# Optimization experiments

Measured on AMD Instinct MI355X. Metric: run time of the kernel, lower is better.

The kernel has to match this reference:

```python
import jax, jax.numpy as jnp
from jax import lax
import numpy as np

D_MODEL = 128
N_HEADS = 8
N_POINTS = 8
MAX_MAG = 10.0
NEG_SLOPE = 0.1


def conv2d(x, w, b, pad):
    # x: (N, Cin, H, W), w: (Cout, Cin, kh, kw)
    y = lax.conv_general_dilated(x, w, (1, 1), [(pad, pad), (pad, pad)],
                                 dimension_numbers=('NCHW', 'OIHW', 'NCHW'))
    return y + b[None, :, None, None]


def leaky(x):
    return jnp.where(x >= 0, x, NEG_SLOPE * x)


def bilinear_sample(img, grid):
    # img: (B, C, H, W); grid: (B, P, H, W, 2) in [-1, 1] (x, y)
    # Matches torch F.grid_sample(mode='bilinear', padding_mode='zeros', align_corners=False)
    B, C, H, W = img.shape
    x = ((grid[..., 0] + 1.0) * W - 1.0) * 0.5
    y = ((grid[..., 1] + 1.0) * H - 1.0) * 0.5
    x0 = jnp.floor(x)
    y0 = jnp.floor(y)
    wx1 = x - x0
    wy1 = y - y0

    def one(img_b, x0b, y0b, wx1b, wy1b):
        def gather(xi, yi):
            valid = (xi >= 0) & (xi < W) & (yi >= 0) & (yi < H)
            xc = jnp.clip(xi, 0, W - 1).astype(jnp.int32)
            yc = jnp.clip(yi, 0, H - 1).astype(jnp.int32)
            v = img_b[:, yc, xc]  # (C, P, H, W)
            return v * valid
        wx0b = 1.0 - wx1b
        wy0b = 1.0 - wy1b
        v00 = gather(x0b, y0b)
        v01 = gather(x0b + 1, y0b)
        v10 = gather(x0b, y0b + 1)
        v11 = gather(x0b + 1, y0b + 1)
        return (v00 * (wx0b * wy0b) + v01 * (wx1b * wy0b)
                + v10 * (wx0b * wy1b) + v11 * (wx1b * wy1b))

    return jax.vmap(one)(img, x0, y0, wx1, wy1)  # (B, C, P, H, W)


def ss_deform_attn(value, loc):
    # value: (N, nh, d, H, W); loc: (N, nh, P, H, W, 2) in normalized [0,1] coords
    N, nh, d, H, W = value.shape
    P = loc.shape[2]
    v = value.reshape(N * nh, d, H, W)
    grids = (2.0 * loc - 1.0).reshape(N * nh, P, H, W, 2)
    sampled = bilinear_sample(v, grids)  # (N*nh, d, P, H, W)
    # per-location attention logits = <sampled_point, value_at_location>
    scores = jnp.einsum('ndphw,ndhw->nphw', sampled, v)
    aw = jax.nn.softmax(scores, axis=1)
    out = jnp.einsum('ndphw,nphw->ndhw', sampled, aw)
    return out.reshape(N, nh * d, H, W)


def _forward(query, value, reference_points, co_w1, co_b1, co_w2, co_b2,
             co_w3, co_b3, co_w4, co_b4, val_w, val_b, out_w, out_b):
    N, C, H, W = value.shape
    v = conv2d(value, val_w, val_b, 0)
    v = v.reshape(N, N_HEADS, D_MODEL // N_HEADS, H, W)
    o = leaky(conv2d(query, co_w1, co_b1, 1))
    o = leaky(conv2d(o, co_w2, co_b2, 1))
    o = leaky(conv2d(o, co_w3, co_b3, 1))
    o = conv2d(o, co_w4, co_b4, 1)
    o = MAX_MAG * jnp.tanh(o)
    offsets = o.reshape(N, N_HEADS, N_POINTS, H, W, 2)
    norm = jnp.array([W, H], dtype=o.dtype)  # (x, y) normalizer
    loc = reference_points[:, None, None, :, :, :] + offsets / norm
    out = ss_deform_attn(v, loc)
    return conv2d(out, out_w, out_b, 0)


def setup_inputs() -> dict:
    key = jax.random.key(0)
    ks = jax.random.split(key, 12)
    N, H, W = 4, 80, 80

    def w_init(k, shape):
        fan_in = shape[1] * shape[2] * shape[3]
        return jax.random.normal(k, shape, jnp.float32) / np.sqrt(fan_in)

    return {
        'query': jax.random.normal(ks[0], (N, 2 * D_MODEL, H, W), jnp.float32),
        'value': jax.random.normal(ks[1], (N, D_MODEL, H, W), jnp.float32),
        'reference_points': jax.random.uniform(ks[2], (N, H, W, 2), jnp.float32),
        'co_w1': w_init(ks[3], (D_MODEL, 2 * D_MODEL, 3, 3)),
        'co_b1': jnp.zeros((D_MODEL,), jnp.float32),
        'co_w2': w_init(ks[4], (D_MODEL, D_MODEL, 3, 3)),
        'co_b2': jnp.zeros((D_MODEL,), jnp.float32),
        'co_w3': w_init(ks[5], (D_MODEL, D_MODEL, 3, 3)),
        'co_b3': jnp.zeros((D_MODEL,), jnp.float32),
        'co_w4': w_init(ks[6], (N_HEADS * N_POINTS * 2, D_MODEL, 3, 3)),
        'co_b4': jnp.zeros((N_HEADS * N_POINTS * 2,), jnp.float32),
        'val_w': w_init(ks[7], (D_MODEL, D_MODEL, 1, 1)),
        'val_b': jnp.zeros((D_MODEL,), jnp.float32),
        'out_w': w_init(ks[8], (D_MODEL, D_MODEL, 1, 1)),
        'out_b': jnp.zeros((D_MODEL,), jnp.float32),
    }


def reference(query, value, reference_points, co_w1, co_b1, co_w2, co_b2,
              co_w3, co_b3, co_w4, co_b4, val_w, val_b, out_w, out_b):
    return _forward(query, value, reference_points, co_w1, co_b1, co_w2, co_b2,
                    co_w3, co_b3, co_w4, co_b4, val_w, val_b, out_w, out_b)
```

## Files before the change

### kernel.cpp

```cpp
#include <hip/hip_runtime.h>
#include <math.h>

#define Hh 80
#define Ww 80
#define HW 6400
#define PS 6724
#define NB 4

typedef _Float16 half8 __attribute__((ext_vector_type(8)));
typedef _Float16 half4v __attribute__((ext_vector_type(4)));
typedef float f32x16 __attribute__((ext_vector_type(16)));

__device__ inline void wblob_one(const float* src, _Float16* dst, int CI, int d) {
    int NC = CI / 32;
    int j = d & 7;
    int l = (d >> 3) & 63;
    int h = (d >> 9) & 1;
    int rest = d >> 10;
    int tap = rest % 9;
    rest /= 9;
    int c = rest % NC;
    int CT = rest / NC;
    int co = CT * 32 + (l & 31);
    int ci = c * 32 + h * 16 + (l >> 5) * 8 + j;
    dst[d] = (_Float16)src[((size_t)co * CI + ci) * 9 + tap];
}

__device__ inline void wblob1x1_one(const float* src, _Float16* dst, int d) {
    int j = d & 7;
    int l = (d >> 3) & 63;
    int c = (d >> 9) & 7;
    int CT = d >> 12;
    int co = CT * 32 + (l & 31);
    int ci = c * 16 + (l >> 5) * 8 + j;
    dst[d] = (_Float16)src[co * 128 + ci];
}

__device__ inline int padsite(int p) {
    if (p < 82) return p;
    if (p < 164) return 81 * 82 + (p - 82);
    if (p < 244) return (p - 163) * 82;
    return (p - 243) * 82 + 81;
}

__global__ void prep_kernel(const float* __restrict__ w1, const float* __restrict__ w2,
                            const float* __restrict__ w3, const float* __restrict__ w4,
                            const float* __restrict__ vw, const float* __restrict__ ow,
                            _Float16* __restrict__ b1, _Float16* __restrict__ b2,
                            _Float16* __restrict__ b3, _Float16* __restrict__ b4,
                            _Float16* __restrict__ bv, _Float16* __restrict__ bo,
                            int* __restrict__ qh_i, int* __restrict__ hA_i,
                            int* __restrict__ hB_i) {
    int idx = blockIdx.x * 256 + threadIdx.x;
    if (idx < 294912) { wblob_one(w1, b1, 256, idx); return; }
    idx -= 294912;
    if (idx < 147456) { wblob_one(w2, b2, 128, idx); return; }
    idx -= 147456;
    if (idx < 147456) { wblob_one(w3, b3, 128, idx); return; }
    idx -= 147456;
    if (idx < 147456) { wblob_one(w4, b4, 128, idx); return; }
    idx -= 147456;
    if (idx < 16384) { wblob1x1_one(vw, bv, idx); return; }
    idx -= 16384;
    if (idx < 16384) { wblob1x1_one(ow, bo, idx); return; }
    idx -= 16384;
    if (idx < 165888) {
        int n = idx / 41472, rr = idx % 41472;
        int c = rr / 5184, r2 = rr % 5184;
        int p = r2 >> 4, k = r2 & 15;
        qh_i[((size_t)(n * 8 + c) * PS + padsite(p)) * 16 + k] = 0;
        return;
    }
    idx -= 165888;
    if (idx < 82944) {
        int n = idx / 20736, rr = idx % 20736;
        int c = rr / 5184, r2 = rr % 5184;
        int p = r2 >> 4, k = r2 & 15;
        hA_i[((size_t)(n * 4 + c) * PS + padsite(p)) * 16 + k] = 0;
        return;
    }
    idx -= 82944;
    if (idx < 82944) {
        int n = idx / 20736, rr = idx % 20736;
        int c = rr / 5184, r2 = rr % 5184;
        int p = r2 >> 4, k = r2 & 15;
        hB_i[((size_t)(n * 4 + c) * PS + padsite(p)) * 16 + k] = 0;
    }
}

__global__ __launch_bounds__(256) void q_transpose(
    const float* __restrict__ in, _Float16* __restrict__ out) {
    const int b = blockIdx.x;
    const int xcd = b & 7, n = xcd & 3, hi = xcd >> 2;
    const int s0 = hi * 3200 + (b >> 3) * 64;
    const int t = threadIdx.x;
    constexpr int CI = 256, ST = CI + 8;
    __shared__ _Float16 T[64 * ST];
    for (int idx = t; idx < 64 * CI; idx += 256) {
        int ci = idx >> 6, sl = idx & 63;
        T[sl * ST + ci] = (_Float16)in[((size_t)n * CI + ci) * HW + s0 + sl];
    }
    __syncthreads();
    for (int idx = t; idx < 64 * 32; idx += 256) {
        int q = idx & 31, sl = idx >> 5;
        int s = s0 + sl, yy = s / 80, xx = s % 80;
        int c = q >> 2, off = (q & 3) * 8;
        *(int4*)(out + ((size_t)(n * 8 + c) * PS + (yy + 1) * 82 + (xx + 1)) * 32 + off) =
            *(const int4*)(&T[sl * ST + q * 8]);
    }
}

__global__ __launch_bounds__(256) void v_transpose(
    const float* __restrict__ in, _Float16* __restrict__ out) {
    const int b = blockIdx.x;
    const int xcd = b & 7, n = xcd & 3, hi = xcd >> 2;
    const int s0 = hi * 3200 + (b >> 3) * 64;
    const int t = threadIdx.x;
    constexpr int CI = 128, ST = CI + 8;
    __shared__ _Float16 T[64 * ST];
    for (int idx = t; idx < 64 * CI; idx += 256) {
        int ci = idx >> 6, sl = idx & 63;
        T[sl * ST + ci] = (_Float16)in[((size_t)n * CI + ci) * HW + s0 + sl];
    }
    __syncthreads();
    for (int idx = t; idx < 64 * 16; idx += 256) {
        int q = idx & 15, sl = idx >> 4;
        *(int4*)(out + ((size_t)n * HW + s0 + sl) * CI + q * 8) =
            *(const int4*)(&T[sl * ST + q * 8]);
    }
}

template <int NCp, int ACT>
__global__ __launch_bounds__(256) void conv3x3_mfma(
    const _Float16* __restrict__ in, const _Float16* __restrict__ wblob,
    const float* __restrict__ bias, void* __restrict__ outp) {
    constexpr int NS = NCp * 18;
    const int b = blockIdx.x;
    const int xcd = b & 7, n = xcd & 3, hi = xcd >> 2;
    const int r = b >> 3;
    const int coH = r & 1, j = r >> 1;
    const int x0 = (j % 5) * 16, y0 = hi * 40 + (j / 5) * 8;
    const int t = threadIdx.x;
    const int w = t >> 6, l = t & 63;
    const int x0w = x0 + (w & 1) * 8, y0w = y0 + (w >> 1) * 4;
    const int lane31 = l & 31, lhalf = l >> 5;
    const int lx = lane31 & 7, ly = lane31 >> 3;

    const _Float16* p0 = in + ((size_t)(n * NCp) * PS + (y0w + ly + 1) * 82 + (x0w + lx + 1)) * 32 + lhalf * 8;
    const _Float16* wA0 = wblob + ((size_t)(coH * 2) * NS) * 512 + l * 8;
    const _Float16* wA1 = wA0 + (size_t)NS * 512;

    f32x16 acc0 = {}, acc1 = {};
    half8 bB[9], bA0[9], bA1[9];

    auto boff = [](int t2) -> size_t {
        int c = t2 / 18, u = t2 % 18;
        int tap = u >> 1, h = u & 1;
        int dy = tap / 3, dx = tap % 3;
        return (size_t)c * (PS * 32) + ((dy - 1) * 82 + (dx - 1)) * 32 + h * 16;
    };

#pragma unroll
    for (int t2 = 0; t2 < 9; ++t2) {
        bB[t2]  = *(const half8*)(p0 + boff(t2));
        bA0[t2] = *(const half8*)(wA0 + t2 * 512);
        bA1[t2] = *(const half8*)(wA1 + t2 * 512);
    }

#pragma unroll
    for (int t2 = 0; t2 < NS; ++t2) {
        const int slot = t2 % 9;
        acc0 = __builtin_amdgcn_mfma_f32_32x32x16_f16(bA0[slot], bB[slot], acc0, 0, 0, 0);
        acc1 = __builtin_amdgcn_mfma_f32_32x32x16_f16(bA1[slot], bB[slot], acc1, 0, 0, 0);
        if (t2 + 9 < NS) {
            const int t2p = t2 + 9;
            bB[slot]  = *(const half8*)(p0 + boff(t2p));
            bA0[slot] = *(const half8*)(wA0 + (size_t)t2p * 512);
            bA1[slot] = *(const half8*)(wA1 + (size_t)t2p * 512);
        }
    }

    const int y = y0w + ly, x = x0w + lx;
#pragma unroll
    for (int ct = 0; ct < 2; ++ct) {
        const f32x16& acc = ct ? acc1 : acc0;
#pragma unroll
        for (int q = 0; q < 4; ++q) {
            const int inner = 8 * q + 4 * lhalf;
            const int co0 = coH * 64 + ct * 32 + inner;
            float v[4];
#pragma unroll
            for (int i = 0; i < 4; ++i) {
                float vv = acc[q * 4 + i] + bias[co0 + i];
                if (ACT == 1) vv = (vv >= 0.f) ? vv : 0.1f * vv;
                else vv = 10.f * tanhf(vv);
                v[i] = vv;
            }
            if (ACT == 1) {
                half4v hv = {(_Float16)v[0], (_Float16)v[1], (_Float16)v[2], (_Float16)v[3]};
                const int c2 = coH * 2 + ct;
                *(half4v*)((_Float16*)outp +
                    ((size_t)(n * 4 + c2) * PS + (y + 1) * 82 + (x + 1)) * 32 + inner) = hv;
            } else {
                float4 fv = {v[0], v[1], v[2], v[3]};
                *(float4*)((float*)outp + ((size_t)n * HW + y * 80 + x) * 128 + co0) = fv;
            }
        }
    }
}

template <int MODE>
__global__ __launch_bounds__(256) void conv1x1_mfma(
    const _Float16* __restrict__ in, const _Float16* __restrict__ wblob,
    const float* __restrict__ bias, float* __restrict__ outp) {
    const int b = blockIdx.x;
    const int xcd = b & 7, n = xcd & 3, hi = xcd >> 2;
    const int r = b >> 3;
    const int coH = r & 1, strip = r >> 1;
    const int t = threadIdx.x;
    const int w = t >> 6, l = t & 63;
    const int lane31 = l & 31, lhalf = l >> 5;
    const int s = hi * 3200 + strip * 128 + w * 32 + lane31;

    const _Float16* pB = in + (size_t)(n * HW + s) * 128 + lhalf * 8;
    const _Float16* pA0 = wblob + (size_t)(coH * 2) * 8 * 512 + l * 8;
    const _Float16* pA1 = pA0 + 8 * 512;

    half8 bB[8], bA0[8], bA1[8];
#pragma unroll
    for (int c = 0; c < 8; ++c) {
        bB[c]  = *(const half8*)(pB + c * 16);
        bA0[c] = *(const half8*)(pA0 + (size_t)c * 512);
        bA1[c] = *(const half8*)(pA1 + (size_t)c * 512);
    }
    f32x16 acc0 = {}, acc1 = {};
#pragma unroll
    for (int c = 0; c < 8; ++c) {
        acc0 = __builtin_amdgcn_mfma_f32_32x32x16_f16(bA0[c], bB[c], acc0, 0, 0, 0);
        acc1 = __builtin_amdgcn_mfma_f32_32x32x16_f16(bA1[c], bB[c], acc1, 0, 0, 0);
    }

#pragma unroll
    for (int ct = 0; ct < 2; ++ct) {
        const f32x16& acc = ct ? acc1 : acc0;
#pragma unroll
        for (int q = 0; q < 4; ++q) {
            const int co0 = coH * 64 + ct * 32 + 8 * q + 4 * lhalf;
            if (MODE == 0) {
                const int hd = co0 >> 4, dd = co0 & 15;
                float4 fv = {acc[4 * q + 0] + bias[co0 + 0], acc[4 * q + 1] + bias[co0 + 1],
                             acc[4 * q + 2] + bias[co0 + 2], acc[4 * q + 3] + bias[co0 + 3]};
                *(float4*)&outp[((size_t)(n * 8 + hd) * HW + s) * 16 + dd] = fv;
            } else {
#pragma unroll
                for (int i = 0; i < 4; ++i)
                    outp[(size_t)(n * 128 + co0 + i) * HW + s] = acc[4 * q + i] + bias[co0 + i];
            }
        }
    }
}

__global__ __launch_bounds__(256, 2) void deform_attn_kernel(
    const float* __restrict__ v_s, const float* __restrict__ offs,
    const float* __restrict__ ref, _Float16* __restrict__ att) {
    const int slice = blockIdx.x;
    const int n = slice >> 3, hd = slice & 7;
    const int t = threadIdx.x;
    const int s = blockIdx.y * 64 + (t >> 2);
    const int d0 = (t & 3) * 4;
    const int nb = n * 8 + hd;
    const float* vbase = v_s + (size_t)nb * (HW * 16) + d0;

    const float4 cv = *(const float4*)&v_s[((size_t)nb * HW + s) * 16 + d0];
    const float rx = ref[(size_t)(n * HW + s) * 2 + 0] * 80.f - 0.5f;
    const float ry = ref[(size_t)(n * HW + s) * 2 + 1] * 80.f - 0.5f;

    const int e = (s >= 3200) ? 1 : 0;
    const float* ob0 = offs + ((size_t)n * HW + (2 * s - e * HW)) * 128 + hd * 16 + e;

    float4 oxv[4], oyv[4];
#pragma unroll
    for (int i = 0; i < 4; ++i) {
        oxv[i] = *(const float4*)(ob0 + i * 4);
        oyv[i] = *(const float4*)(ob0 + 128 + i * 4);
    }
    float ox[8], oy[8];
#pragma unroll
    for (int i = 0; i < 4; ++i) {
        ox[2 * i] = oxv[i].x; ox[2 * i + 1] = oxv[i].z;
        oy[2 * i] = oyv[i].x; oy[2 * i + 1] = oyv[i].z;
    }

    float wx1[8], wy1[8];
    int ix[8], iy[8];
#pragma unroll
    for (int p = 0; p < 8; ++p) {
        const float px = rx + ox[p];
        const float py = ry + oy[p];
        const float fx = floorf(px), fy = floorf(py);
        ix[p] = (int)fx; iy[p] = (int)fy;
        wx1[p] = px - fx; wy1[p] = py - fy;
    }

    float4 g[8][4];
#pragma unroll
    for (int p = 0; p < 8; ++p) {
        const int xc0 = min(max(ix[p], 0), 79),     xc1 = min(max(ix[p] + 1, 0), 79);
        const int yc0 = min(max(iy[p], 0), 79),     yc1 = min(max(iy[p] + 1, 0), 79);
        const int r0 = yc0 * 80, r1 = yc1 * 80;
        g[p][0] = *(const float4*)(vbase + (size_t)(r0 + xc0) * 16);
        g[p][1] = *(const float4*)(vbase + (size_t)(r0 + xc1) * 16);
        g[p][2] = *(const float4*)(vbase + (size_t)(r1 + xc0) * 16);
        g[p][3] = *(const float4*)(vbase + (size_t)(r1 + xc1) * 16);
    }

    float4 sampled[8];
    float score[8];
#pragma unroll
    for (int p = 0; p < 8; ++p) {
        const float vx0 = (ix[p] >= 0 && ix[p] < Ww) ? 1.f : 0.f;
        const float vx1 = (ix[p] + 1 >= 0 && ix[p] + 1 < Ww) ? 1.f : 0.f;
        const float vy0 = (iy[p] >= 0 && iy[p] < Hh) ? 1.f : 0.f;
        const float vy1 = (iy[p] + 1 >= 0 && iy[p] + 1 < Hh) ? 1.f : 0.f;
        const float wx0 = 1.f - wx1[p], wy0 = 1.f - wy1[p];
        const float w00 = wx0 * wy0 * vx0 * vy0;
        const float w01 = wx1[p] * wy0 * vx1 * vy0;
        const float w10 = wx0 * wy1[p] * vx0 * vy1;
        const float w11 = wx1[p] * wy1[p] * vx1 * vy1;
        float4 sv;
        sv.x = g[p][0].x * w00 + g[p][1].x * w01 + g[p][2].x * w10 + g[p][3].x * w11;
        sv.y = g[p][0].y * w00 + g[p][1].y * w01 + g[p][2].y * w10 + g[p][3].y * w11;
        sv.z = g[p][0].z * w00 + g[p][1].z * w01 + g[p][2].z * w10 + g[p][3].z * w11;
        sv.w = g[p][0].w * w00 + g[p][1].w * w01 + g[p][2].w * w10 + g[p][3].w * w11;
        sampled[p] = sv;
        float sc = sv.x * cv.x + sv.y * cv.y + sv.z * cv.z + sv.w * cv.w;
        sc += __shfl_xor(sc, 1);
        sc += __shfl_xor(sc, 2);
        score[p] = sc;
    }

    float m = score[0];
#pragma unroll
    for (int p = 1; p < 8; ++p) m = fmaxf(m, score[p]);
    float sum = 0.f, aw[8];
#pragma unroll
    for (int p = 0; p < 8; ++p) {
        aw[p] = __expf(score[p] - m);
        sum += aw[p];
    }
    const float inv = 1.f / sum;
    float4 o = {0.f, 0.f, 0.f, 0.f};
#pragma unroll
    for (int p = 0; p < 8; ++p) {
        o.x += aw[p] * sampled[p].x;
        o.y += aw[p] * sampled[p].y;
        o.z += aw[p] * sampled[p].z;
        o.w += aw[p] * sampled[p].w;
    }
    o.x *= inv; o.y *= inv; o.z *= inv; o.w *= inv;

    half4v hv = {(_Float16)o.x, (_Float16)o.y, (_Float16)o.z, (_Float16)o.w};
    *(half4v*)&att[((size_t)n * HW + s) * 128 + hd * 16 + d0] = hv;
}

extern "C" void kernel_launch(void* const* d_in, const int* in_sizes, int n_in,
                              void* d_out, int out_size, void* d_ws, size_t ws_size,
                              hipStream_t stream) {
    const float* query = (const float*)d_in[0];
    const float* value = (const float*)d_in[1];
    const float* ref   = (const float*)d_in[2];
    const float* co_w1 = (const float*)d_in[3];
    const float* co_b1 = (const float*)d_in[4];
    const float* co_w2 = (const float*)d_in[5];
    const float* co_b2 = (const float*)d_in[6];
    const float* co_w3 = (const float*)d_in[7];
    const float* co_b3 = (const float*)d_in[8];
    const float* co_w4 = (const float*)d_in[9];
    const float* co_b4 = (const float*)d_in[10];
    const float* val_w = (const float*)d_in[11];
    const float* val_b = (const float*)d_in[12];
    const float* out_w = (const float*)d_in[13];
    const float* out_b = (const float*)d_in[14];

    char* ws = (char*)d_ws;
    size_t o = 0;
    auto alloc = [&](size_t bytes) { char* p = ws + o; o += (bytes + 255) & ~(size_t)255; return p; };

    _Float16* wb2 = (_Float16*)alloc(147456 * 2);
    _Float16* wb3 = (_Float16*)alloc(147456 * 2);
    _Float16* wb4 = (_Float16*)alloc(147456 * 2);
    _Float16* wbv = (_Float16*)alloc(16384 * 2);
    _Float16* wbo = (_Float16*)alloc(16384 * 2);
    char* vsR = alloc(3276800 * 4);
    float* v_s = (float*)vsR;
    _Float16* wb1 = (_Float16*)vsR;
    _Float16* v_h = (_Float16*)alloc((size_t)NB * HW * 128 * 2);
    char* R1 = alloc((size_t)NB * 8 * PS * 32 * 2);
    _Float16* q_h = (_Float16*)R1;
    float* o4 = (float*)R1;
    char* R2 = alloc((size_t)NB * 4 * PS * 32 * 2 * 2);
    _Float16* hA = (_Float16*)R2;
    _Float16* hB = (_Float16*)(R2 + (size_t)NB * 4 * PS * 32 * 2);
    _Float16* att_h = (_Float16*)R2;

    prep_kernel<<<4304, 256, 0, stream>>>(co_w1, co_w2, co_w3, co_w4, val_w, out_w,
                                          wb1, wb2, wb3, wb4, wbv, wbo,
                                          (int*)q_h, (int*)hA, (int*)hB);

    q_transpose<<<400, 256, 0, stream>>>(query, q_h);
    v_transpose<<<400, 256, 0, stream>>>(value, v_h);

    conv3x3_mfma<8, 1><<<400, 256, 0, stream>>>(q_h, wb1, co_b1, hA);

    conv1x1_mfma<0><<<400, 256, 0, stream>>>(v_h, wbv, val_b, v_s);

    conv3x3_mfma<4, 1><<<400, 256, 0, stream>>>(hA, wb2, co_b2, hB);
    conv3x3_mfma<4, 1><<<400, 256, 0, stream>>>(hB, wb3, co_b3, hA);
    conv3x3_mfma<4, 2><<<400, 256, 0, stream>>>(hA, wb4, co_b4, o4);

    deform_attn_kernel<<<dim3(32, 100), 256, 0, stream>>>(v_s, o4, ref, att_h);

    conv1x1_mfma<1><<<400, 256, 0, stream>>>(att_h, wbo, out_b, (float*)d_out);
}
```

Baseline: 266.9 us.

## Stage conv3x3 weights and input halo in LDS via async global_load_lds double-buffering

Restructures the 3x3 conv MFMA kernel so each block covers all 128 output channels for a 16x4 pixel tile. Weights and a halo'd input tile are staged into shared memory with direct global-to-LDS loads, double-buffered per channel group. Previously each wave loaded its operands straight from global memory into registers, which meant redundant input reads across the split output-channel halves. The change adds LDS traffic and a barrier per tap group, and sets a two-blocks-per-CU occupancy hint.

```diff
diff --git a/kernel.cpp b/kernel.cpp
--- a/kernel.cpp
+++ b/kernel.cpp
@@ -10,6 +10,12 @@
 typedef _Float16 half8 __attribute__((ext_vector_type(8)));
 typedef _Float16 half4v __attribute__((ext_vector_type(4)));
 typedef float f32x16 __attribute__((ext_vector_type(16)));
+
+__device__ __forceinline__ void gload16(const _Float16* g, _Float16* l) {
+    __builtin_amdgcn_global_load_lds(
+        (const __attribute__((address_space(1))) void*)g,
+        (__attribute__((address_space(3))) void*)l, 16, 0, 0);
+}
 
 __device__ inline void wblob_one(const float* src, _Float16* dst, int CI, int d) {
     int NC = CI / 32;
@@ -131,63 +137,92 @@
 }
 
 template <int NCp, int ACT>
-__global__ __launch_bounds__(256) void conv3x3_mfma(
+__global__ __launch_bounds__(256, 2) void conv3x3_mfma(
     const _Float16* __restrict__ in, const _Float16* __restrict__ wblob,
     const float* __restrict__ bias, void* __restrict__ outp) {
     constexpr int NS = NCp * 18;
+    constexpr int NG = NCp * 3;
+    __shared__ _Float16 Abuf[2][24 * 512];
+    __shared__ _Float16 Bbuf[2][6 * 1024];
+
     const int b = blockIdx.x;
     const int xcd = b & 7, n = xcd & 3, hi = xcd >> 2;
     const int r = b >> 3;
-    const int coH = r & 1, j = r >> 1;
-    const int x0 = (j % 5) * 16, y0 = hi * 40 + (j / 5) * 8;
+    const int x0 = (r % 5) * 16, y0 = hi * 40 + (r / 5) * 4;
     const int t = threadIdx.x;
     const int w = t >> 6, l = t & 63;
-    const int x0w = x0 + (w & 1) * 8, y0w = y0 + (w >> 1) * 4;
     const int lane31 = l & 31, lhalf = l >> 5;
-    const int lx = lane31 & 7, ly = lane31 >> 3;
-
-    const _Float16* p0 = in + ((size_t)(n * NCp) * PS + (y0w + ly + 1) * 82 + (x0w + lx + 1)) * 32 + lhalf * 8;
-    const _Float16* wA0 = wblob + ((size_t)(coH * 2) * NS) * 512 + l * 8;
-    const _Float16* wA1 = wA0 + (size_t)NS * 512;
+    const int lx = lane31 & 15, lyw = lane31 >> 4;
+    const int si = l & 15, g8 = l >> 4;
+
+    const _Float16* bplane0 = in + (size_t)(n * NCp) * PS * 32;
+    const _Float16* wA = wblob + (size_t)w * NS * 512 + l * 8;
 
     f32x16 acc0 = {}, acc1 = {};
-    half8 bB[9], bA0[9], bA1[9];
-
-    auto boff = [](int t2) -> size_t {
-        int c = t2 / 18, u = t2 % 18;
-        int tap = u >> 1, h = u & 1;
-        int dy = tap / 3, dx = tap % 3;
-        return (size_t)c * (PS * 32) + ((dy - 1) * 82 + (dx - 1)) * 32 + h * 16;
-    };
-
-#pragma unroll
-    for (int t2 = 0; t2 < 9; ++t2) {
-        bB[t2]  = *(const half8*)(p0 + boff(t2));
-        bA0[t2] = *(const half8*)(wA0 + t2 * 512);
-        bA1[t2] = *(const half8*)(wA1 + t2 * 512);
-    }
-
-#pragma unroll
-    for (int t2 = 0; t2 < NS; ++t2) {
-        const int slot = t2 % 9;
-        acc0 = __builtin_amdgcn_mfma_f32_32x32x16_f16(bA0[slot], bB[slot], acc0, 0, 0, 0);
-        acc1 = __builtin_amdgcn_mfma_f32_32x32x16_f16(bA1[slot], bB[slot], acc1, 0, 0, 0);
-        if (t2 + 9 < NS) {
-            const int t2p = t2 + 9;
-            bB[slot]  = *(const half8*)(p0 + boff(t2p));
-            bA0[slot] = *(const half8*)(wA0 + (size_t)t2p * 512);
-            bA1[slot] = *(const half8*)(wA1 + (size_t)t2p * 512);
+
+#pragma unroll
+    for (int k2 = 0; k2 < 6; ++k2)
+        gload16(wA + (size_t)k2 * 512, &Abuf[0][(k2 * 4 + w) * 512]);
+#pragma unroll
+    for (int j = 0; j < 3; ++j) {
+        const int m = 3 * w + j, rr = m >> 1, sg = m & 1;
+        gload16(bplane0 + ((size_t)((y0 + rr) * 82 + x0 + sg * 16 + si)) * 32 + g8 * 8,
+                &Bbuf[0][rr * 1024 + sg * 512]);
+    }
+    __syncthreads();
+
+    const _Float16* bplane = bplane0;
+#pragma unroll 1
+    for (int c = 0; c < NCp; ++c) {
+        const _Float16* bplaneN = bplane + (size_t)PS * 32;
+        const int cpar = c & 1;
+#pragma unroll
+        for (int gi = 0; gi < 3; ++gi) {
+            const int grp = c * 3 + gi;
+            if (grp + 1 < NG) {
+                const _Float16* asrc = wA + (size_t)(grp + 1) * 6 * 512;
+                _Float16* adst = &Abuf[(grp + 1) & 1][w * 512];
+#pragma unroll
+                for (int k2 = 0; k2 < 6; ++k2)
+                    gload16(asrc + (size_t)k2 * 512, adst + k2 * 4 * 512);
+            }
+            if (gi == 2 && c + 1 < NCp) {
+#pragma unroll
+                for (int j = 0; j < 3; ++j) {
+                    const int m = 3 * w + j, rr = m >> 1, sg = m & 1;
+                    gload16(bplaneN + ((size_t)((y0 + rr) * 82 + x0 + sg * 16 + si)) * 32 + g8 * 8,
+                            &Bbuf[(c + 1) & 1][rr * 1024 + sg * 512]);
+                }
+            }
+            const _Float16* ab = Abuf[grp & 1];
+            const _Float16* bb = Bbuf[cpar];
+#pragma unroll
+            for (int k = 0; k < 6; ++k) {
+                const int u = gi * 6 + k;
+                const int tap = u >> 1, h = u & 1;
+                const int dy = tap / 3, dx = tap % 3;
+                half8 a = *(const half8*)&ab[(k * 4 + w) * 512 + l * 8];
+                const int cx = lx + dx;
+                const int boff = (cx >> 4) * 512 + (h * 2 + lhalf) * 128 + (cx & 15) * 8;
+                half8 b0 = *(const half8*)&bb[(lyw + dy) * 1024 + boff];
+                half8 b1 = *(const half8*)&bb[(lyw + 2 + dy) * 1024 + boff];
+                acc0 = __builtin_amdgcn_mfma_f32_32x32x16_f16(a, b0, acc0, 0, 0, 0);
+                acc1 = __builtin_amdgcn_mfma_f32_32x32x16_f16(a, b1, acc1, 0, 0, 0);
+            }
+            __syncthreads();
         }
-    }
-
-    const int y = y0w + ly, x = x0w + lx;
-#pragma unroll
-    for (int ct = 0; ct < 2; ++ct) {
-        const f32x16& acc = ct ? acc1 : acc0;
+        bplane = bplaneN;
+    }
+
+    const int x = x0 + lx;
+#pragma unroll
+    for (int f = 0; f < 2; ++f) {
+        const f32x16& acc = f ? acc1 : acc0;
+        const int y = y0 + lyw + 2 * f;
 #pragma unroll
         for (int q = 0; q < 4; ++q) {
             const int inner = 8 * q + 4 * lhalf;
-            const int co0 = coH * 64 + ct * 32 + inner;
+            const int co0 = w * 32 + inner;
             float v[4];
 #pragma unroll
             for (int i = 0; i < 4; ++i) {
@@ -198,9 +233,8 @@
             }
             if (ACT == 1) {
                 half4v hv = {(_Float16)v[0], (_Float16)v[1], (_Float16)v[2], (_Float16)v[3]};
-                const int c2 = coH * 2 + ct;
                 *(half4v*)((_Float16*)outp +
-                    ((size_t)(n * 4 + c2) * PS + (y + 1) * 82 + (x + 1)) * 32 + inner) = hv;
+                    ((size_t)(n * 4 + w) * PS + (y + 1) * 82 + (x + 1)) * 32 + inner) = hv;
             } else {
                 float4 fv = {v[0], v[1], v[2], v[3]};
                 *(float4*)((float*)outp + ((size_t)n * HW + y * 80 + x) * 128 + co0) = fv;
```

After: 238.6 us. -10.6%, faster.
